# Kernel optimization log

Measured on AMD Instinct MI355X. Metric: run time of the kernel, lower is better.

## Reference

```python
import jax, jax.numpy as jnp
import numpy as np

EPS = 1e-10
COMMITMENT_COST = 0.25


def setup_inputs() -> dict:
    key = jax.random.key(0)
    kx, kw = jax.random.split(key)
    B, H, W, D, K = 32, 32, 32, 256, 8192
    x = jax.random.normal(kx, (B, H, W, D), dtype=jnp.float32)
    # codebook initialized RandomUniform(-1, 1), shape [embedding_dim, n_embeddings]
    w = jax.random.uniform(kw, (D, K), dtype=jnp.float32, minval=-1.0, maxval=1.0)
    return {"x": x, "w": w, "is_training": 1}


def reference(x, w, is_training):
    D, K = w.shape
    flat_x = x.reshape(-1, D)  # [N, D]
    distances = (
        jnp.sum(flat_x * flat_x, axis=1, keepdims=True)
        - 2.0 * (flat_x @ w)
        + jnp.sum(w * w, axis=0, keepdims=True)
    )
    encoding_indices_flat = jnp.argmin(distances, axis=1)  # [N]
    encodings = jax.nn.one_hot(encoding_indices_flat, K, dtype=x.dtype)  # [N, K]
    encoding_indices = encoding_indices_flat.reshape(x.shape[:-1])  # [B, H, W]
    quantized = jnp.take(w.T, encoding_indices, axis=0)  # [B, H, W, D]

    e_latent_loss = jnp.mean((jax.lax.stop_gradient(quantized) - x) ** 2)
    q_latent_loss = jnp.mean((quantized - jax.lax.stop_gradient(x)) ** 2)
    loss = q_latent_loss + COMMITMENT_COST * e_latent_loss

    # straight-through estimator
    quantized_st = x + jax.lax.stop_gradient(quantized - x)

    avg_probs = jnp.mean(encodings, axis=0)  # [K]
    perplexity = jnp.exp(-jnp.sum(avg_probs * jnp.log(avg_probs + EPS)))

    return quantized_st, loss, perplexity, encodings, encoding_indices
```

## Files before the change

### kernel.cpp

```cpp
#include <hip/hip_runtime.h>
#include <math.h>

typedef _Float16 f16x8 __attribute__((ext_vector_type(8)));
typedef float f32x4 __attribute__((ext_vector_type(4)));

#define N_PTS 32768
#define DIM 256
#define K_CODES 8192
#define NSTRIP 4
#define SCOLS 2048
#define NCT 16

#define WS_WNH     0
#define WS_COUNTS  32768
#define WS_LOSSP   65536
#define WS_PART    262144
#define WS_WT      2359296
#define WS_BPK     10747904

#define GLL(dst, src) __builtin_amdgcn_global_load_lds( \
    (const __attribute__((address_space(1))) void*)(src), \
    (__attribute__((address_space(3))) void*)(dst), 16, 0, 0)

__global__ void vq_prep(const float* __restrict__ w, float* __restrict__ wnh,
                        int* __restrict__ counts) {
    int k = blockIdx.x * 256 + threadIdx.x;
    double s0 = 0.0, s1 = 0.0, s2 = 0.0, s3 = 0.0;
    for (int d = 0; d < DIM; d += 4) {
        float a = w[(size_t)d * K_CODES + k];
        float b = w[(size_t)(d + 1) * K_CODES + k];
        float c = w[(size_t)(d + 2) * K_CODES + k];
        float e = w[(size_t)(d + 3) * K_CODES + k];
        s0 += (double)a * a; s1 += (double)b * b;
        s2 += (double)c * c; s3 += (double)e * e;
    }
    wnh[k] = (float)(0.5 * ((s0 + s1) + (s2 + s3)));
    counts[k] = 0;
}

__global__ void vq_prep_w(const float* __restrict__ w, char* __restrict__ Bpk,
                          float* __restrict__ wT) {
    __shared__ float t[64][129];
    int tid = threadIdx.x;
    int ct = blockIdx.x >> 2, ks4 = blockIdx.x & 3;
    int k0 = ks4 * 64, n0 = ct * 128;
    for (int i = 0; i < 32; ++i) {
        int idx = i * 256 + tid;
        int kk = idx >> 7, nn = idx & 127;
        t[kk][nn] = w[(size_t)(k0 + kk) * K_CODES + n0 + nn];
    }
    __syncthreads();
    for (int i = 0; i < 4; ++i) {
        int c = i * 256 + tid;
        int nn = c >> 3, k8 = c & 7;
        f16x8 hi;
#pragma unroll
        for (int e = 0; e < 8; ++e) hi[e] = (_Float16)t[k8 * 8 + e][nn];
        int off = nn * 128 + ((k8 ^ (nn & 7)) << 4);
        *(f16x8*)(Bpk + (((size_t)blockIdx.x) << 14) + off) = hi;
    }
    for (int i = 0; i < 32; ++i) {
        int idx = i * 256 + tid;
        int nn = idx >> 6, kk = idx & 63;
        wT[(size_t)(n0 + nn) * DIM + k0 + kk] = t[kk][nn];
    }
}

__global__ __launch_bounds__(256, 2)
void vq_mfma(const float* __restrict__ x, const char* __restrict__ Bpk,
             const float* __restrict__ wnh, float4* __restrict__ part) {
    __shared__ __align__(16) char Bs[2][16384];
    __shared__ float wnhs[2048];

    const int tid = threadIdx.x;
    const int lane = tid & 63;
    const int wid = tid >> 6;
    const int l15 = lane & 15, l4 = lane >> 4;
    const int bid = blockIdx.x;
    const int strip = (bid & 7) >> 1;
    const int mblk = (bid >> 3) | ((bid & 1) << 7);

    for (int i = tid; i < 2048; i += 256) wnhs[i] = wnh[strip * 2048 + i];

    f16x8 a[2][4][2];
#pragma unroll
    for (int m = 0; m < 2; ++m) {
        const float* xr = x + (size_t)(mblk * 128 + wid * 32 + m * 16 + l15) * DIM;
#pragma unroll
        for (int kp = 0; kp < 4; ++kp)
#pragma unroll
            for (int kk = 0; kk < 2; ++kk) {
                const float* p = xr + kp * 64 + (kk * 4 + l4) * 8;
                float4 u = *(const float4*)p, v = *(const float4*)(p + 4);
                f16x8 h;
                h[0] = (_Float16)u.x; h[1] = (_Float16)u.y;
                h[2] = (_Float16)u.z; h[3] = (_Float16)u.w;
                h[4] = (_Float16)v.x; h[5] = (_Float16)v.y;
                h[6] = (_Float16)v.z; h[7] = (_Float16)v.w;
                a[m][kp][kk] = h;
            }
    }

    int bB[2];
    bB[0] = l15 * 128 + ((l4 ^ (l15 & 7)) << 4);
    bB[1] = l15 * 128 + (((4 + l4) ^ (l15 & 7)) << 4);

    float v1[8], v2[8];
    int i1[8], i2[8];
#pragma unroll
    for (int r = 0; r < 8; ++r) {
        v1[r] = INFINITY; v2[r] = INFINITY;
        i1[r] = 0x7fffffff; i2[r] = 0x7fffffff;
    }

    const int t16 = tid << 4;
    const char* bbase = Bpk + (((size_t)strip * 64) << 14);

#pragma unroll
    for (int q = 0; q < 4; ++q) GLL(Bs[0] + q * 4096 + t16, bbase + q * 4096 + t16);
    __syncthreads();

    for (int ct = 0; ct < NCT; ++ct) {
        f32x4 acc[2][8];
#pragma unroll
        for (int m = 0; m < 2; ++m)
#pragma unroll
            for (int n = 0; n < 8; ++n)
#pragma unroll
                for (int e = 0; e < 4; ++e) acc[m][n][e] = 0.f;

#pragma unroll
        for (int kp = 0; kp < 4; ++kp) {
            const int cur = kp & 1;
            const int s = ct * 4 + kp;
            if (s < 63) {
                const char* src = bbase + ((size_t)(s + 1) << 14);
#pragma unroll
                for (int q = 0; q < 4; ++q)
                    GLL(Bs[cur ^ 1] + q * 4096 + t16, src + q * 4096 + t16);
            }
#pragma unroll
            for (int kk = 0; kk < 2; ++kk) {
#pragma unroll
                for (int n = 0; n < 8; ++n) {
                    f16x8 b = *(const f16x8*)(&Bs[cur][bB[kk] + n * 2048]);
                    acc[0][n] = __builtin_amdgcn_mfma_f32_16x16x32_f16(
                        a[0][kp][kk], b, acc[0][n], 0, 0, 0);
                    acc[1][n] = __builtin_amdgcn_mfma_f32_16x16x32_f16(
                        a[1][kp][kk], b, acc[1][n], 0, 0, 0);
                }
            }
            if (kp == 3) {
#pragma unroll
                for (int n = 0; n < 8; ++n) {
                    const int cl = ct * 128 + n * 16 + l15;
                    const float wv = wnhs[cl];
                    const int k = strip * SCOLS + cl;
#pragma unroll
                    for (int m = 0; m < 2; ++m)
#pragma unroll
                        for (int j = 0; j < 4; ++j) {
                            const int r = m * 4 + j;
                            float v = wv - acc[m][n][j];
                            bool lt1 = v < v1[r];
                            bool lt2 = v < v2[r];
                            float tv = lt2 ? v : v2[r];
                            int ti = lt2 ? k : i2[r];
                            v2[r] = lt1 ? v1[r] : tv;
                            i2[r] = lt1 ? i1[r] : ti;
                            v1[r] = lt1 ? v : v1[r];
                            i1[r] = lt1 ? k : i1[r];
                        }
                }
            }
            __syncthreads();
        }
    }

#pragma unroll
    for (int mask = 1; mask <= 8; mask <<= 1) {
#pragma unroll
        for (int r = 0; r < 8; ++r) {
            float ov1 = __shfl_xor(v1[r], mask); int oi1 = __shfl_xor(i1[r], mask);
            float ov2 = __shfl_xor(v2[r], mask); int oi2 = __shfl_xor(i2[r], mask);
            bool fa = (v1[r] < ov1) || (v1[r] == ov1 && i1[r] < oi1);
            float nv1 = fa ? v1[r] : ov1; int ni1 = fa ? i1[r] : oi1;
            float cs = fa ? ov1 : v1[r]; int ci = fa ? oi1 : i1[r];
            float ws_ = fa ? v2[r] : ov2; int wi = fa ? i2[r] : oi2;
            bool sb = (cs < ws_) || (cs == ws_ && ci < wi);
            v1[r] = nv1; i1[r] = ni1;
            v2[r] = sb ? cs : ws_; i2[r] = sb ? ci : wi;
        }
    }
    if (l15 == 0) {
#pragma unroll
        for (int m = 0; m < 2; ++m)
#pragma unroll
            for (int j = 0; j < 4; ++j) {
                int r = m * 4 + j;
                int row = mblk * 128 + wid * 32 + m * 16 + l4 * 4 + j;
                part[(size_t)strip * N_PTS + row] =
                    make_float4(v1[r], __int_as_float(i1[r]), v2[r], __int_as_float(i2[r]));
            }
    }
}

__global__ void vq_rerank(const float4* __restrict__ part, const float* __restrict__ x,
                          const float* __restrict__ wT, int* __restrict__ counts,
                          float* __restrict__ out_idx, float* __restrict__ out_enc,
                          float* __restrict__ outq, float* __restrict__ lossPart) {
    const int lane = threadIdx.x & 63;
    const int row = blockIdx.x * 4 + (threadIdx.x >> 6);

    float v = INFINITY;
    int ii = 0x7fffffff;
    if (lane < 8) {
        float4 p = part[(size_t)(lane >> 1) * N_PTS + row];
        v = (lane & 1) ? p.z : p.x;
        ii = __float_as_int((lane & 1) ? p.w : p.y);
    }
    int sel0, sel1, sel2;
#pragma unroll
    for (int t = 0; t < 3; ++t) {
        float mv = v; int mi = ii;
#pragma unroll
        for (int mask = 1; mask <= 4; mask <<= 1) {
            float ov = __shfl_xor(mv, mask); int oi = __shfl_xor(mi, mask);
            if (ov < mv || (ov == mv && oi < mi)) { mv = ov; mi = oi; }
        }
        int win = __shfl(mi, 0);
        if (t == 0) sel0 = win; else if (t == 1) sel1 = win; else sel2 = win;
        if (ii == win) v = INFINITY;
    }
    const int grp = lane >> 4;
    int cnd = sel0;
    if (grp == 1) cnd = sel1;
    if (grp == 2) cnd = sel2;
    const int d0 = (lane & 15) * 16;
    const float* xp = x + (size_t)row * DIM + d0;
    const float* wp = wT + (size_t)cnd * DIM + d0;
    double s = 0.0;
#pragma unroll
    for (int q = 0; q < 4; ++q) {
        float4 xa = *(const float4*)(xp + q * 4);
        float4 wa = *(const float4*)(wp + q * 4);
        double dx;
        dx = (double)xa.x - (double)wa.x; s += dx * dx;
        dx = (double)xa.y - (double)wa.y; s += dx * dx;
        dx = (double)xa.z - (double)wa.z; s += dx * dx;
        dx = (double)xa.w - (double)wa.w; s += dx * dx;
    }
#pragma unroll
    for (int mask = 1; mask <= 8; mask <<= 1) s += __shfl_xor(s, mask);
    double dA = __shfl(s, 0), dB = __shfl(s, 16), dC = __shfl(s, 32);
    double bd = dA; int bi = sel0;
    if (dB < bd || (dB == bd && sel1 < bi)) { bd = dB; bi = sel1; }
    if (dC < bd || (dC == bd && sel2 < bi)) { bd = dC; bi = sel2; }
    const int best = bi;

    if (lane == 0) {
        out_idx[row] = (float)best;
        out_enc[(size_t)row * K_CODES + best] = 1.0f;
        atomicAdd(&counts[best], 1);
    }
    float4 xq = *(const float4*)(x + (size_t)row * DIM + lane * 4);
    float4 wq = *(const float4*)(wT + (size_t)best * DIM + lane * 4);
    *(float4*)(outq + (size_t)row * DIM + lane * 4) = wq;
    float d1 = wq.x - xq.x, d2 = wq.y - xq.y, d3 = wq.z - xq.z, d4 = wq.w - xq.w;
    float ls = d1 * d1 + d2 * d2 + d3 * d3 + d4 * d4;

    __shared__ float red[256];
    red[threadIdx.x] = ls;
    __syncthreads();
    for (int m = 128; m > 0; m >>= 1) {
        if (threadIdx.x < m) red[threadIdx.x] += red[threadIdx.x + m];
        __syncthreads();
    }
    if (threadIdx.x == 0) lossPart[blockIdx.x] = red[0];
}

__global__ void vq_final(const int* __restrict__ counts, const float* __restrict__ lossPart,
                         float* __restrict__ out_loss, float* __restrict__ out_perp) {
    __shared__ float red[256];
    __shared__ float red2[256];
    int tid = threadIdx.x;
    float h = 0.f;
    for (int k = tid; k < K_CODES; k += 256) {
        float p = (float)counts[k] * (1.0f / N_PTS);
        h += p * logf(p + 1e-10f);
    }
    float l = 0.f;
    for (int k = tid; k < 8192; k += 256) l += lossPart[k];
    red[tid] = h;
    red2[tid] = l;
    __syncthreads();
    for (int m = 128; m > 0; m >>= 1) {
        if (tid < m) { red[tid] += red[tid + m]; red2[tid] += red2[tid + m]; }
        __syncthreads();
    }
    if (tid == 0) {
        *out_perp = expf(-red[0]);
        *out_loss = 1.25f * red2[0] / 8388608.0f;
    }
}

extern "C" void kernel_launch(void* const* d_in, const int* in_sizes, int n_in,
                              void* d_out, int out_size, void* d_ws, size_t ws_size,
                              hipStream_t stream) {
    const float* x = (const float*)d_in[0];
    const float* w = (const float*)d_in[1];

    float* outf = (float*)d_out;
    float* outq = outf;
    float* out_loss = outf + (size_t)8388608;
    float* out_perp = outf + (size_t)8388609;
    float* out_enc = outf + (size_t)8388610;
    float* out_idx = outf + (size_t)8388610 + (size_t)268435456;

    char* wsb = (char*)d_ws;
    float* wnh = (float*)(wsb + WS_WNH);
    int* counts = (int*)(wsb + WS_COUNTS);
    float* lossPart = (float*)(wsb + WS_LOSSP);
    float4* part = (float4*)(wsb + WS_PART);
    float* wT = (float*)(wsb + WS_WT);
    char* Bpk = wsb + WS_BPK;

    vq_prep<<<dim3(32), dim3(256), 0, stream>>>(w, wnh, counts);
    vq_prep_w<<<dim3(256), dim3(256), 0, stream>>>(w, Bpk, wT);

    vq_mfma<<<dim3(1024), dim3(256), 0, stream>>>(x, Bpk, wnh, part);

    vq_rerank<<<dim3(8192), dim3(256), 0, stream>>>(part, x, wT, counts,
                                                    out_idx, out_enc, outq, lossPart);
    vq_final<<<dim3(1), dim3(256), 0, stream>>>(counts, lossPart, out_loss, out_perp);
}
```

Baseline: 246.4 us.

## Pre-convert x to fp16 and double MFMA block size to share codebook tiles

Adds a prep kernel that converts x to a packed fp16 buffer so the MFMA kernel loads A fragments directly. The MFMA kernel now runs 512-thread blocks covering 256 rows, so each LDS codebook tile is shared by twice as many waves, halving total codebook streaming. It also changes block-to-strip mapping and drops to one block per CU occupancy; the extra prep kernel adds a full read/write pass over x.

```diff
diff --git a/kernel.cpp b/kernel.cpp
--- a/kernel.cpp
+++ b/kernel.cpp
@@ -17,6 +17,7 @@
 #define WS_PART    262144
 #define WS_WT      2359296
 #define WS_BPK     10747904
+#define WS_XPK     14942208
 
 #define GLL(dst, src) __builtin_amdgcn_global_load_lds( \
     (const __attribute__((address_space(1))) void*)(src), \
@@ -38,6 +39,19 @@
     counts[k] = 0;
 }
 
+__global__ void vq_prep_x(const float* __restrict__ x, _Float16* __restrict__ xpk) {
+    int gid = blockIdx.x * 256 + threadIdx.x;
+    int r = gid >> 5, kc = gid & 31;
+    const float* xp = x + (size_t)r * DIM + kc * 8;
+    float4 u = *(const float4*)xp, v = *(const float4*)(xp + 4);
+    f16x8 h;
+    h[0] = (_Float16)u.x; h[1] = (_Float16)u.y;
+    h[2] = (_Float16)u.z; h[3] = (_Float16)u.w;
+    h[4] = (_Float16)v.x; h[5] = (_Float16)v.y;
+    h[6] = (_Float16)v.z; h[7] = (_Float16)v.w;
+    *(f16x8*)(xpk + (size_t)r * DIM + kc * 8) = h;
+}
+
 __global__ void vq_prep_w(const float* __restrict__ w, char* __restrict__ Bpk,
                           float* __restrict__ wT) {
     __shared__ float t[64][129];
@@ -66,8 +80,8 @@
     }
 }
 
-__global__ __launch_bounds__(256, 2)
-void vq_mfma(const float* __restrict__ x, const char* __restrict__ Bpk,
+__global__ __launch_bounds__(512, 1)
+void vq_mfma(const _Float16* __restrict__ xpk, const char* __restrict__ Bpk,
              const float* __restrict__ wnh, float4* __restrict__ part) {
     __shared__ __align__(16) char Bs[2][16384];
     __shared__ float wnhs[2048];
@@ -77,28 +91,20 @@
     const int wid = tid >> 6;
     const int l15 = lane & 15, l4 = lane >> 4;
     const int bid = blockIdx.x;
-    const int strip = (bid & 7) >> 1;
-    const int mblk = (bid >> 3) | ((bid & 1) << 7);
-
-    for (int i = tid; i < 2048; i += 256) wnhs[i] = wnh[strip * 2048 + i];
+    const int strip = bid >> 7;
+    const int mblk = bid & 127;
+
+    for (int i = tid; i < 2048; i += 512) wnhs[i] = wnh[strip * 2048 + i];
 
     f16x8 a[2][4][2];
 #pragma unroll
     for (int m = 0; m < 2; ++m) {
-        const float* xr = x + (size_t)(mblk * 128 + wid * 32 + m * 16 + l15) * DIM;
+        const _Float16* xr = xpk + (size_t)(mblk * 256 + wid * 32 + m * 16 + l15) * DIM;
 #pragma unroll
         for (int kp = 0; kp < 4; ++kp)
 #pragma unroll
-            for (int kk = 0; kk < 2; ++kk) {
-                const float* p = xr + kp * 64 + (kk * 4 + l4) * 8;
-                float4 u = *(const float4*)p, v = *(const float4*)(p + 4);
-                f16x8 h;
-                h[0] = (_Float16)u.x; h[1] = (_Float16)u.y;
-                h[2] = (_Float16)u.z; h[3] = (_Float16)u.w;
-                h[4] = (_Float16)v.x; h[5] = (_Float16)v.y;
-                h[6] = (_Float16)v.z; h[7] = (_Float16)v.w;
-                a[m][kp][kk] = h;
-            }
+            for (int kk = 0; kk < 2; ++kk)
+                a[m][kp][kk] = *(const f16x8*)(xr + kp * 64 + kk * 32 + l4 * 8);
     }
 
     int bB[2];
@@ -116,8 +122,8 @@
     const int t16 = tid << 4;
     const char* bbase = Bpk + (((size_t)strip * 64) << 14);
 
-#pragma unroll
-    for (int q = 0; q < 4; ++q) GLL(Bs[0] + q * 4096 + t16, bbase + q * 4096 + t16);
+    GLL(Bs[0] + t16, bbase + t16);
+    GLL(Bs[0] + 8192 + t16, bbase + 8192 + t16);
     __syncthreads();
 
     for (int ct = 0; ct < NCT; ++ct) {
@@ -135,9 +141,8 @@
             const int s = ct * 4 + kp;
             if (s < 63) {
                 const char* src = bbase + ((size_t)(s + 1) << 14);
-#pragma unroll
-                for (int q = 0; q < 4; ++q)
-                    GLL(Bs[cur ^ 1] + q * 4096 + t16, src + q * 4096 + t16);
+                GLL(Bs[cur ^ 1] + t16, src + t16);
+                GLL(Bs[cur ^ 1] + 8192 + t16, src + 8192 + t16);
             }
 #pragma unroll
             for (int kk = 0; kk < 2; ++kk) {
@@ -198,7 +203,7 @@
 #pragma unroll
             for (int j = 0; j < 4; ++j) {
                 int r = m * 4 + j;
-                int row = mblk * 128 + wid * 32 + m * 16 + l4 * 4 + j;
+                int row = mblk * 256 + wid * 32 + m * 16 + l4 * 4 + j;
                 part[(size_t)strip * N_PTS + row] =
                     make_float4(v1[r], __int_as_float(i1[r]), v2[r], __int_as_float(i2[r]));
             }
@@ -324,11 +329,13 @@
     float4* part = (float4*)(wsb + WS_PART);
     float* wT = (float*)(wsb + WS_WT);
     char* Bpk = wsb + WS_BPK;
+    _Float16* xpk = (_Float16*)(wsb + WS_XPK);
 
     vq_prep<<<dim3(32), dim3(256), 0, stream>>>(w, wnh, counts);
+    vq_prep_x<<<dim3(4096), dim3(256), 0, stream>>>(x, xpk);
     vq_prep_w<<<dim3(256), dim3(256), 0, stream>>>(w, Bpk, wT);
 
-    vq_mfma<<<dim3(1024), dim3(256), 0, stream>>>(x, Bpk, wnh, part);
+    vq_mfma<<<dim3(512), dim3(512), 0, stream>>>(xpk, Bpk, wnh, part);
 
     vq_rerank<<<dim3(8192), dim3(256), 0, stream>>>(part, x, wT, counts,
                                                     out_idx, out_enc, outq, lossPart);
```

Measured after the change: 276.5 us. 1.12x slower.
